# Optimization experiments

Hardware: AMD Instinct MI355X
Metric: run time of the kernel (lower is better)

## Reference

```python
import jax, jax.numpy as jnp
import numpy as np

D_IN, D_BIAS, H, DH = 256, 128, 8, 32

def _layernorm(x, w, b, eps=1e-5):
    mu = jnp.mean(x, axis=-1, keepdims=True)
    var = jnp.var(x, axis=-1, keepdims=True)
    return (x - mu) * jax.lax.rsqrt(var + eps) * w + b

def setup_inputs() -> dict:
    key = jax.random.key(0)
    ks = jax.random.split(key, 8)
    B, L = 1, 768
    x = jax.random.normal(ks[0], (B, L, D_IN), dtype=jnp.float32)
    bias = jax.random.normal(ks[1], (B, L, L, D_BIAS), dtype=jnp.float32)
    s_in = 1.0 / np.sqrt(D_IN)
    s_b = 1.0 / np.sqrt(D_BIAS)
    return {
        "x": x,
        "bias": bias,
        "ln_in_w": jnp.ones((D_IN,), jnp.float32),
        "ln_in_b": jnp.zeros((D_IN,), jnp.float32),
        "ln_b_w": jnp.ones((D_BIAS,), jnp.float32),
        "ln_b_b": jnp.zeros((D_BIAS,), jnp.float32),
        "Wq": jax.random.normal(ks[2], (D_IN, H * DH), jnp.float32) * s_in,
        "Wk": jax.random.normal(ks[3], (D_IN, H * DH), jnp.float32) * s_in,
        "Wv": jax.random.normal(ks[4], (D_IN, H * DH), jnp.float32) * s_in,
        "Wb": jax.random.normal(ks[5], (D_BIAS, H), jnp.float32) * s_b,
        "Wg": jax.random.normal(ks[6], (D_IN, H * DH), jnp.float32) * 0.02,
        "bg": jnp.ones((H * DH,), jnp.float32),
        "Wo": jax.random.normal(ks[7], (H * DH, D_IN), jnp.float32) * 0.02,
        "bo": jnp.zeros((D_IN,), jnp.float32),
    }

def reference(x, bias, ln_in_w, ln_in_b, ln_b_w, ln_b_b, Wq, Wk, Wv, Wb, Wg, bg, Wo, bo):
    B, L, _ = x.shape
    scaling = 1.0 / np.sqrt(DH)
    xn = _layernorm(x, ln_in_w, ln_in_b)            # (B,L,D_IN)
    bn = _layernorm(bias, ln_b_w, ln_b_b)           # (B,L,L,D_BIAS)
    q = (xn @ Wq).reshape(B, L, H, DH)
    k = (xn @ Wk).reshape(B, L, H, DH) * scaling
    v = (xn @ Wv).reshape(B, L, H, DH)
    b = bn @ Wb                                     # (B,L,L,H)
    gate = jax.nn.sigmoid(xn @ Wg + bg)             # (B,L,H*DH)
    attn = jnp.einsum('bqhd,bkhd->bqkh', q, k) + b  # (B,q,k,h)
    attn = jax.nn.softmax(attn, axis=2)             # softmax over key dim
    out = jnp.einsum('bqkh,bkhd->bqhd', attn, v).reshape(B, L, H * DH)
    out = gate * out
    return out @ Wo + bo
```

## Files before the change

### kernel.cpp

```cpp
#include <hip/hip_runtime.h>

#define LQ 768
#define DIN 256
#define DB 128
#define NH 8
#define DH 32

#define OFF_QB 0
#define OFF_KB (LQ*DIN)
#define OFF_VB (2*LQ*DIN)
#define OFF_GB (3*LQ*DIN)
#define OFF_W2 (4*LQ*DIN)
#define OFF_SC (OFF_W2 + DB*NH)
#define OFF_QK (OFF_SC + 16)

__global__ __launch_bounds__(256) void projsetup_kernel(
    const float* __restrict__ x, const float* __restrict__ lnw, const float* __restrict__ lnb,
    const float* __restrict__ Wq, const float* __restrict__ Wk, const float* __restrict__ Wv,
    const float* __restrict__ Wg, const float* __restrict__ bg,
    const float* __restrict__ lbw, const float* __restrict__ lbb, const float* __restrict__ Wb,
    float* __restrict__ qb, float* __restrict__ kb, float* __restrict__ vb, float* __restrict__ gb,
    float* __restrict__ W2, float* __restrict__ SC)
{
    const int tid = threadIdx.x;

    if (blockIdx.x == 192) {
        if (tid < 128) {
            const int d = tid, lane = d & 63, wv = d >> 6;
            float w = lbw[d], b = lbb[d];
            float pS[NH], pC[NH];
            #pragma unroll
            for (int h = 0; h < NH; h++) {
                float wb = Wb[d*NH + h];
                float w2 = w * wb;
                W2[d*NH + h] = w2;
                pS[h] = w2;
                pC[h] = b * wb;
            }
            #pragma unroll
            for (int m = 1; m <= 32; m <<= 1) {
                #pragma unroll
                for (int h = 0; h < NH; h++) { pS[h] += __shfl_xor(pS[h], m); pC[h] += __shfl_xor(pC[h], m); }
            }
            __shared__ float red[2][16];
            if (lane == 0) {
                #pragma unroll
                for (int h = 0; h < NH; h++) { red[wv][h] = pS[h]; red[wv][NH+h] = pC[h]; }
            }
            __syncthreads();
            if (d < 16) SC[d] = red[0][d] + red[1][d];
        }
        return;
    }

    const int lane = tid & 63, rr = tid >> 6;
    const int row = blockIdx.x * 4 + rr;
    __shared__ float xn[4][DIN];

    float4 xv = ((const float4*)x)[row * (DIN/4) + lane];
    float s  = xv.x + xv.y + xv.z + xv.w;
    float ss = xv.x*xv.x + xv.y*xv.y + xv.z*xv.z + xv.w*xv.w;
    #pragma unroll
    for (int m = 1; m <= 32; m <<= 1) { s += __shfl_xor(s, m); ss += __shfl_xor(ss, m); }
    float mu  = s * (1.0f/DIN);
    float inv = rsqrtf(ss * (1.0f/DIN) - mu*mu + 1e-5f);
    float4 wv4 = ((const float4*)lnw)[lane];
    float4 bv4 = ((const float4*)lnb)[lane];
    float4 r4;
    r4.x = (xv.x - mu)*inv*wv4.x + bv4.x;
    r4.y = (xv.y - mu)*inv*wv4.y + bv4.y;
    r4.z = (xv.z - mu)*inv*wv4.z + bv4.z;
    r4.w = (xv.w - mu)*inv*wv4.w + bv4.w;
    *((float4*)&xn[rr][lane*4]) = r4;
    __syncthreads();

    const int col = tid;
    float aq[4] = {0,0,0,0}, ak[4] = {0,0,0,0}, av[4] = {0,0,0,0}, ag[4] = {0,0,0,0};
    for (int i4 = 0; i4 < DIN/4; i4++) {
        float4 x0 = *((const float4*)&xn[0][i4*4]);
        float4 x1 = *((const float4*)&xn[1][i4*4]);
        float4 x2 = *((const float4*)&xn[2][i4*4]);
        float4 x3 = *((const float4*)&xn[3][i4*4]);
        const float* p0 = (const float*)&x0;
        const float* p1 = (const float*)&x1;
        const float* p2 = (const float*)&x2;
        const float* p3 = (const float*)&x3;
        #pragma unroll
        for (int e = 0; e < 4; e++) {
            const int i = i4*4 + e;
            float wq = Wq[i*DIN + col], wk = Wk[i*DIN + col];
            float wvv = Wv[i*DIN + col], wg = Wg[i*DIN + col];
            aq[0] = fmaf(p0[e], wq, aq[0]); aq[1] = fmaf(p1[e], wq, aq[1]);
            aq[2] = fmaf(p2[e], wq, aq[2]); aq[3] = fmaf(p3[e], wq, aq[3]);
            ak[0] = fmaf(p0[e], wk, ak[0]); ak[1] = fmaf(p1[e], wk, ak[1]);
            ak[2] = fmaf(p2[e], wk, ak[2]); ak[3] = fmaf(p3[e], wk, ak[3]);
            av[0] = fmaf(p0[e], wvv, av[0]); av[1] = fmaf(p1[e], wvv, av[1]);
            av[2] = fmaf(p2[e], wvv, av[2]); av[3] = fmaf(p3[e], wvv, av[3]);
            ag[0] = fmaf(p0[e], wg, ag[0]); ag[1] = fmaf(p1[e], wg, ag[1]);
            ag[2] = fmaf(p2[e], wg, ag[2]); ag[3] = fmaf(p3[e], wg, ag[3]);
        }
    }
    const float kscale = 0.17677669529663687f;
    float bgv = bg[col];
    #pragma unroll
    for (int r = 0; r < 4; r++) {
        const int orow = blockIdx.x*4 + r;
        qb[orow*DIN + col] = aq[r];
        kb[orow*DIN + col] = ak[r] * kscale;
        vb[orow*DIN + col] = av[r];
        gb[orow*DIN + col] = 1.0f/(1.0f + __expf(-(ag[r] + bgv)));
    }
}

__global__ __launch_bounds__(256) void qk_kernel(
    const float* __restrict__ qb, const float* __restrict__ kb, float* __restrict__ qkT)
{
    __shared__ float q_l[32*260];
    __shared__ float k_l[32*260];
    const int tid = threadIdx.x;
    const int bq = blockIdx.x, bk = blockIdx.y;

    {
        const int row = tid >> 3, cg = tid & 7;
        const float4* qs = (const float4*)(qb + (size_t)(bq*32 + row)*DIN + cg*32);
        const float4* ks = (const float4*)(kb + (size_t)(bk*32 + row)*DIN + cg*32);
        #pragma unroll
        for (int j = 0; j < 8; j++) {
            *(float4*)&q_l[row*260 + cg*32 + j*4] = qs[j];
            *(float4*)&k_l[row*260 + cg*32 + j*4] = ks[j];
        }
    }
    __syncthreads();

    const int tx = tid & 15, ty = tid >> 4;
    float acc[2][2][NH];
    #pragma unroll
    for (int a = 0; a < 2; a++)
        #pragma unroll
        for (int b = 0; b < 2; b++)
            #pragma unroll
            for (int h = 0; h < NH; h++) acc[a][b][h] = 0.f;

    #pragma unroll
    for (int d4 = 0; d4 < 64; d4++) {
        const int h = d4 >> 3;
        float4 q0 = *(const float4*)&q_l[(ty*2+0)*260 + d4*4];
        float4 q1 = *(const float4*)&q_l[(ty*2+1)*260 + d4*4];
        float4 k0 = *(const float4*)&k_l[(tx*2+0)*260 + d4*4];
        float4 k1 = *(const float4*)&k_l[(tx*2+1)*260 + d4*4];
        acc[0][0][h] = fmaf(q0.x,k0.x,acc[0][0][h]); acc[0][0][h] = fmaf(q0.y,k0.y,acc[0][0][h]);
        acc[0][0][h] = fmaf(q0.z,k0.z,acc[0][0][h]); acc[0][0][h] = fmaf(q0.w,k0.w,acc[0][0][h]);
        acc[0][1][h] = fmaf(q0.x,k1.x,acc[0][1][h]); acc[0][1][h] = fmaf(q0.y,k1.y,acc[0][1][h]);
        acc[0][1][h] = fmaf(q0.z,k1.z,acc[0][1][h]); acc[0][1][h] = fmaf(q0.w,k1.w,acc[0][1][h]);
        acc[1][0][h] = fmaf(q1.x,k0.x,acc[1][0][h]); acc[1][0][h] = fmaf(q1.y,k0.y,acc[1][0][h]);
        acc[1][0][h] = fmaf(q1.z,k0.z,acc[1][0][h]); acc[1][0][h] = fmaf(q1.w,k0.w,acc[1][0][h]);
        acc[1][1][h] = fmaf(q1.x,k1.x,acc[1][1][h]); acc[1][1][h] = fmaf(q1.y,k1.y,acc[1][1][h]);
        acc[1][1][h] = fmaf(q1.z,k1.z,acc[1][1][h]); acc[1][1][h] = fmaf(q1.w,k1.w,acc[1][1][h]);
    }

    #pragma unroll
    for (int a = 0; a < 2; a++)
        #pragma unroll
        for (int b = 0; b < 2; b++) {
            size_t base = ((size_t)(bq*32 + ty*2 + a)*LQ + (bk*32 + tx*2 + b))*NH;
            *(float4*)(qkT + base)     = make_float4(acc[a][b][0], acc[a][b][1], acc[a][b][2], acc[a][b][3]);
            *(float4*)(qkT + base + 4) = make_float4(acc[a][b][4], acc[a][b][5], acc[a][b][6], acc[a][b][7]);
        }
}

__global__ __launch_bounds__(256, 2) void fused_kernel(
    const float* __restrict__ bias, const float* __restrict__ W2g,
    const float* __restrict__ SCg, const float* __restrict__ qkT,
    const float* __restrict__ vbuf, const float* __restrict__ gbuf,
    const float* __restrict__ Wo, const float* __restrict__ bo,
    float* __restrict__ out)
{
    __shared__ float pT[NH][776];
    __shared__ float ao[DIN];
    __shared__ float isum[NH];

    const int tid  = threadIdx.x;
    const int q    = blockIdx.x;
    const int key8 = tid >> 3;
    const int dseg = tid & 7;

    float w2r[16][NH];
    {
        const float4* wp = (const float4*)(W2g + dseg*16*NH);
        #pragma unroll
        for (int j = 0; j < 16; j++) {
            float4 a = wp[j*2], b = wp[j*2+1];
            w2r[j][0]=a.x; w2r[j][1]=a.y; w2r[j][2]=a.z; w2r[j][3]=a.w;
            w2r[j][4]=b.x; w2r[j][5]=b.y; w2r[j][6]=b.z; w2r[j][7]=b.w;
        }
    }
    float Sh[NH], Ch[NH];
    #pragma unroll
    for (int h = 0; h < NH; h++) { Sh[h] = SCg[h]; Ch[h] = SCg[NH+h]; }

    const float* bsrc = bias + (size_t)q*LQ*DB + key8*DB + dseg*16;
    const float* qksrc = qkT + (size_t)q*LQ*NH + key8*NH + dseg;

    float4 va[4], vb4[4];

    #define LOADT(dst, t) {                                         \
        const float4* p = (const float4*)(bsrc + (size_t)(t)*4096); \
        dst[0]=p[0]; dst[1]=p[1]; dst[2]=p[2]; dst[3]=p[3]; }

    #define PROCESS(v, ht) {                                                    \
        float qk = qksrc[(ht)*32*NH];                                           \
        float s = 0.f, ss = 0.f;                                                \
        float acc[NH] = {0,0,0,0,0,0,0,0};                                      \
        _Pragma("unroll")                                                       \
        for (int j = 0; j < 4; j++) {                                           \
            _Pragma("unroll")                                                   \
            for (int e = 0; e < 4; e++) {                                       \
                float xv = (&v[j].x)[e];                                        \
                s += xv; ss = fmaf(xv, xv, ss);                                 \
                _Pragma("unroll")                                               \
                for (int h = 0; h < NH; h++)                                    \
                    acc[h] = fmaf(xv, w2r[j*4+e][h], acc[h]);                   \
            }                                                                   \
        }                                                                       \
        _Pragma("unroll")                                                       \
        for (int m = 1; m <= 4; m <<= 1) {                                      \
            s += __shfl_xor(s, m); ss += __shfl_xor(ss, m);                     \
            _Pragma("unroll")                                                   \
            for (int h = 0; h < NH; h++) acc[h] += __shfl_xor(acc[h], m);       \
        }                                                                       \
        float ah = acc[0], shh = Sh[0], chh = Ch[0];                            \
        _Pragma("unroll")                                                       \
        for (int h = 1; h < NH; h++) {                                          \
            bool psel = (dseg == h);                                            \
            ah = psel ? acc[h] : ah; shh = psel ? Sh[h] : shh;                  \
            chh = psel ? Ch[h] : chh;                                           \
        }                                                                       \
        float mu2  = s * (1.0f/DB);                                             \
        float inv2 = rsqrtf(ss * (1.0f/DB) - mu2*mu2 + 1e-5f);                  \
        float lo = fmaf(inv2, fmaf(-mu2, shh, ah), chh) + qk;                   \
        pT[dseg][(ht)*32 + key8] = lo; }

    LOADT(va, 0);
    for (int hp = 0; hp < 12; hp++) {
        LOADT(vb4, 2*hp + 1);
        PROCESS(va, 2*hp);
        if (hp < 11) LOADT(va, 2*hp + 2);
        PROCESS(vb4, 2*hp + 1);
    }
    #undef LOADT
    #undef PROCESS
    __syncthreads();

    {
        const int h = tid >> 5, l = tid & 31;
        float m = -1e30f;
        for (int i = l; i < LQ; i += 32) m = fmaxf(m, pT[h][i]);
        #pragma unroll
        for (int mm = 1; mm <= 16; mm <<= 1) m = fmaxf(m, __shfl_xor(m, mm));
        float sum = 0.f;
        for (int i = l; i < LQ; i += 32) {
            float e = __expf(pT[h][i] - m);
            pT[h][i] = e;
            sum += e;
        }
        #pragma unroll
        for (int mm = 1; mm <= 16; mm <<= 1) sum += __shfl_xor(sum, mm);
        if (l == 0) isum[h] = 1.0f / sum;
    }
    __syncthreads();

    {
        const int h = tid >> 5, d = tid & 31;
        const float* vp = vbuf + h*DH + d;
        float a = 0.f;
        for (int k4 = 0; k4 < LQ/4; k4++) {
            float4 p = *(const float4*)&pT[h][k4*4];
            a = fmaf(p.x, vp[(size_t)(k4*4+0)*DIN], a);
            a = fmaf(p.y, vp[(size_t)(k4*4+1)*DIN], a);
            a = fmaf(p.z, vp[(size_t)(k4*4+2)*DIN], a);
            a = fmaf(p.w, vp[(size_t)(k4*4+3)*DIN], a);
        }
        ao[tid] = a * isum[h] * gbuf[(size_t)q*DIN + tid];
    }
    __syncthreads();

    {
        float o = bo[tid];
        for (int i = 0; i < DIN; i++) o = fmaf(ao[i], Wo[i*DIN + tid], o);
        out[(size_t)q*DIN + tid] = o;
    }
}

extern "C" void kernel_launch(void* const* d_in, const int* in_sizes, int n_in,
                              void* d_out, int out_size, void* d_ws, size_t ws_size,
                              hipStream_t stream) {
    const float* x    = (const float*)d_in[0];
    const float* bias = (const float*)d_in[1];
    const float* lnw  = (const float*)d_in[2];
    const float* lnb  = (const float*)d_in[3];
    const float* lbw  = (const float*)d_in[4];
    const float* lbb  = (const float*)d_in[5];
    const float* Wq   = (const float*)d_in[6];
    const float* Wk   = (const float*)d_in[7];
    const float* Wv   = (const float*)d_in[8];
    const float* Wb   = (const float*)d_in[9];
    const float* Wg   = (const float*)d_in[10];
    const float* bg   = (const float*)d_in[11];
    const float* Wo   = (const float*)d_in[12];
    const float* bo   = (const float*)d_in[13];

    float* ws = (float*)d_ws;
    float* qb = ws + OFF_QB;
    float* kb = ws + OFF_KB;
    float* vb = ws + OFF_VB;
    float* gb = ws + OFF_GB;
    float* W2 = ws + OFF_W2;
    float* SC = ws + OFF_SC;
    float* qk = ws + OFF_QK;

    projsetup_kernel<<<193, 256, 0, stream>>>(x, lnw, lnb, Wq, Wk, Wv, Wg, bg,
                                              lbw, lbb, Wb, qb, kb, vb, gb, W2, SC);
    qk_kernel<<<dim3(24, 24), 256, 0, stream>>>(qb, kb, qk);
    fused_kernel<<<LQ, 256, 0, stream>>>(bias, W2, SC, qk, vb, gb, Wo, bo, (float*)d_out);
}
```

Before: 180.9 us.

## Fuse QK computation into main kernel and stage bias tiles through swizzled LDS

The separate qk_kernel and its global qkT buffer are removed. Each query block now computes its own row of Q·K scores from a transposed K buffer that the projection kernel writes. The bias layernorm/projection loop is restructured so each wave stages 16-key bias tiles into XOR-swizzled shared memory, prefetching the next tile in registers. W2 moves from registers to shared memory and the reduction is done across lane groups. This removes one launch and the qkT round trip through global memory, and should cut register pressure. The cost is more LDS traffic and extra per-block QK work, which re-reads the whole K matrix for every query.

```diff
diff --git a/kernel.cpp b/kernel.cpp
--- a/kernel.cpp
+++ b/kernel.cpp
@@ -7,19 +7,18 @@
 #define DH 32
 
 #define OFF_QB 0
-#define OFF_KB (LQ*DIN)
+#define OFF_KT (LQ*DIN)
 #define OFF_VB (2*LQ*DIN)
 #define OFF_GB (3*LQ*DIN)
 #define OFF_W2 (4*LQ*DIN)
 #define OFF_SC (OFF_W2 + DB*NH)
-#define OFF_QK (OFF_SC + 16)
 
 __global__ __launch_bounds__(256) void projsetup_kernel(
     const float* __restrict__ x, const float* __restrict__ lnw, const float* __restrict__ lnb,
     const float* __restrict__ Wq, const float* __restrict__ Wk, const float* __restrict__ Wv,
     const float* __restrict__ Wg, const float* __restrict__ bg,
     const float* __restrict__ lbw, const float* __restrict__ lbb, const float* __restrict__ Wb,
-    float* __restrict__ qb, float* __restrict__ kb, float* __restrict__ vb, float* __restrict__ gb,
+    float* __restrict__ qb, float* __restrict__ kT, float* __restrict__ vb, float* __restrict__ gb,
     float* __restrict__ W2, float* __restrict__ SC)
 {
     const int tid = threadIdx.x;
@@ -106,150 +105,143 @@
     for (int r = 0; r < 4; r++) {
         const int orow = blockIdx.x*4 + r;
         qb[orow*DIN + col] = aq[r];
-        kb[orow*DIN + col] = ak[r] * kscale;
         vb[orow*DIN + col] = av[r];
         gb[orow*DIN + col] = 1.0f/(1.0f + __expf(-(ag[r] + bgv)));
     }
+    *((float4*)&kT[col*LQ + blockIdx.x*4]) =
+        make_float4(ak[0]*kscale, ak[1]*kscale, ak[2]*kscale, ak[3]*kscale);
 }
 
-__global__ __launch_bounds__(256) void qk_kernel(
-    const float* __restrict__ qb, const float* __restrict__ kb, float* __restrict__ qkT)
+__global__ __launch_bounds__(256) void mega_kernel(
+    const float* __restrict__ bias, const float* __restrict__ W2g,
+    const float* __restrict__ SCg, const float* __restrict__ qbuf,
+    const float* __restrict__ kT, const float* __restrict__ vbuf,
+    const float* __restrict__ gbuf, const float* __restrict__ Wo,
+    const float* __restrict__ bo, float* __restrict__ out)
 {
-    __shared__ float q_l[32*260];
-    __shared__ float k_l[32*260];
-    const int tid = threadIdx.x;
-    const int bq = blockIdx.x, bk = blockIdx.y;
-
-    {
-        const int row = tid >> 3, cg = tid & 7;
-        const float4* qs = (const float4*)(qb + (size_t)(bq*32 + row)*DIN + cg*32);
-        const float4* ks = (const float4*)(kb + (size_t)(bk*32 + row)*DIN + cg*32);
-        #pragma unroll
-        for (int j = 0; j < 8; j++) {
-            *(float4*)&q_l[row*260 + cg*32 + j*4] = qs[j];
-            *(float4*)&k_l[row*260 + cg*32 + j*4] = ks[j];
-        }
-    }
-    __syncthreads();
-
-    const int tx = tid & 15, ty = tid >> 4;
-    float acc[2][2][NH];
-    #pragma unroll
-    for (int a = 0; a < 2; a++)
-        #pragma unroll
-        for (int b = 0; b < 2; b++)
-            #pragma unroll
-            for (int h = 0; h < NH; h++) acc[a][b][h] = 0.f;
-
-    #pragma unroll
-    for (int d4 = 0; d4 < 64; d4++) {
-        const int h = d4 >> 3;
-        float4 q0 = *(const float4*)&q_l[(ty*2+0)*260 + d4*4];
-        float4 q1 = *(const float4*)&q_l[(ty*2+1)*260 + d4*4];
-        float4 k0 = *(const float4*)&k_l[(tx*2+0)*260 + d4*4];
-        float4 k1 = *(const float4*)&k_l[(tx*2+1)*260 + d4*4];
-        acc[0][0][h] = fmaf(q0.x,k0.x,acc[0][0][h]); acc[0][0][h] = fmaf(q0.y,k0.y,acc[0][0][h]);
-        acc[0][0][h] = fmaf(q0.z,k0.z,acc[0][0][h]); acc[0][0][h] = fmaf(q0.w,k0.w,acc[0][0][h]);
-        acc[0][1][h] = fmaf(q0.x,k1.x,acc[0][1][h]); acc[0][1][h] = fmaf(q0.y,k1.y,acc[0][1][h]);
-        acc[0][1][h] = fmaf(q0.z,k1.z,acc[0][1][h]); acc[0][1][h] = fmaf(q0.w,k1.w,acc[0][1][h]);
-        acc[1][0][h] = fmaf(q1.x,k0.x,acc[1][0][h]); acc[1][0][h] = fmaf(q1.y,k0.y,acc[1][0][h]);
-        acc[1][0][h] = fmaf(q1.z,k0.z,acc[1][0][h]); acc[1][0][h] = fmaf(q1.w,k0.w,acc[1][0][h]);
-        acc[1][1][h] = fmaf(q1.x,k1.x,acc[1][1][h]); acc[1][1][h] = fmaf(q1.y,k1.y,acc[1][1][h]);
-        acc[1][1][h] = fmaf(q1.z,k1.z,acc[1][1][h]); acc[1][1][h] = fmaf(q1.w,k1.w,acc[1][1][h]);
-    }
-
-    #pragma unroll
-    for (int a = 0; a < 2; a++)
-        #pragma unroll
-        for (int b = 0; b < 2; b++) {
-            size_t base = ((size_t)(bq*32 + ty*2 + a)*LQ + (bk*32 + tx*2 + b))*NH;
-            *(float4*)(qkT + base)     = make_float4(acc[a][b][0], acc[a][b][1], acc[a][b][2], acc[a][b][3]);
-            *(float4*)(qkT + base + 4) = make_float4(acc[a][b][4], acc[a][b][5], acc[a][b][6], acc[a][b][7]);
-        }
-}
-
-__global__ __launch_bounds__(256, 2) void fused_kernel(
-    const float* __restrict__ bias, const float* __restrict__ W2g,
-    const float* __restrict__ SCg, const float* __restrict__ qkT,
-    const float* __restrict__ vbuf, const float* __restrict__ gbuf,
-    const float* __restrict__ Wo, const float* __restrict__ bo,
-    float* __restrict__ out)
-{
+    __shared__ float tiles[4][2048];
+    __shared__ float w2p[4*264];
     __shared__ float pT[NH][776];
     __shared__ float ao[DIN];
     __shared__ float isum[NH];
 
     const int tid  = threadIdx.x;
     const int q    = blockIdx.x;
-    const int key8 = tid >> 3;
-    const int dseg = tid & 7;
-
-    float w2r[16][NH];
-    {
-        const float4* wp = (const float4*)(W2g + dseg*16*NH);
-        #pragma unroll
-        for (int j = 0; j < 16; j++) {
-            float4 a = wp[j*2], b = wp[j*2+1];
-            w2r[j][0]=a.x; w2r[j][1]=a.y; w2r[j][2]=a.z; w2r[j][3]=a.w;
-            w2r[j][4]=b.x; w2r[j][5]=b.y; w2r[j][6]=b.z; w2r[j][7]=b.w;
-        }
-    }
+    const int w    = tid >> 6;
+    const int lane = tid & 63;
+    const int key  = lane & 15;
+    const int q4   = lane >> 4;
+
+    const char* gwave = (const char*)bias + ((size_t)q*LQ + w*192) * (DB*4);
+    float* tw = &tiles[w][0];
+
+    int soff[8];
+    #pragma unroll
+    for (int c = 0; c < 8; c++) {
+        int L = c*1024 + lane*16;
+        soff[c] = L ^ (((L >> 9) & 15) << 4);
+    }
+
+    float4 v[8];
+    #pragma unroll
+    for (int c = 0; c < 8; c++) v[c] = *(const float4*)(gwave + soff[c]);
+
+    for (int j = tid; j < 4*264; j += 256) {
+        int g = j / 264, rem = j - g*264;
+        w2p[j] = (rem < 256) ? W2g[g*256 + rem] : 0.0f;
+    }
+
+    if (tid < 192) {
+        float acc[4][NH];
+        #pragma unroll
+        for (int e = 0; e < 4; e++)
+            #pragma unroll
+            for (int h = 0; h < NH; h++) acc[e][h] = 0.f;
+        const float* qp = qbuf + (size_t)q*DIN;
+        #pragma unroll
+        for (int h = 0; h < NH; h++) {
+            #pragma unroll
+            for (int dd = 0; dd < DH; dd++) {
+                const int d = h*DH + dd;
+                float4 kv = *(const float4*)(kT + (size_t)d*LQ + tid*4);
+                float qa = qp[d];
+                acc[0][h] = fmaf(qa, kv.x, acc[0][h]);
+                acc[1][h] = fmaf(qa, kv.y, acc[1][h]);
+                acc[2][h] = fmaf(qa, kv.z, acc[2][h]);
+                acc[3][h] = fmaf(qa, kv.w, acc[3][h]);
+            }
+        }
+        #pragma unroll
+        for (int h = 0; h < NH; h++)
+            *(float4*)&pT[h][tid*4] = make_float4(acc[0][h], acc[1][h], acc[2][h], acc[3][h]);
+    }
+
+    asm volatile("s_waitcnt lgkmcnt(0)" ::: "memory");
+    __builtin_amdgcn_s_barrier();
+    asm volatile("" ::: "memory");
+
     float Sh[NH], Ch[NH];
     #pragma unroll
-    for (int h = 0; h < NH; h++) { Sh[h] = SCg[h]; Ch[h] = SCg[NH+h]; }
-
-    const float* bsrc = bias + (size_t)q*LQ*DB + key8*DB + dseg*16;
-    const float* qksrc = qkT + (size_t)q*LQ*NH + key8*NH + dseg;
-
-    float4 va[4], vb4[4];
-
-    #define LOADT(dst, t) {                                         \
-        const float4* p = (const float4*)(bsrc + (size_t)(t)*4096); \
-        dst[0]=p[0]; dst[1]=p[1]; dst[2]=p[2]; dst[3]=p[3]; }
-
-    #define PROCESS(v, ht) {                                                    \
-        float qk = qksrc[(ht)*32*NH];                                           \
-        float s = 0.f, ss = 0.f;                                                \
-        float acc[NH] = {0,0,0,0,0,0,0,0};                                      \
-        _Pragma("unroll")                                                       \
-        for (int j = 0; j < 4; j++) {                                           \
-            _Pragma("unroll")                                                   \
-            for (int e = 0; e < 4; e++) {                                       \
-                float xv = (&v[j].x)[e];                                        \
-                s += xv; ss = fmaf(xv, xv, ss);                                 \
-                _Pragma("unroll")                                               \
-                for (int h = 0; h < NH; h++)                                    \
-                    acc[h] = fmaf(xv, w2r[j*4+e][h], acc[h]);                   \
-            }                                                                   \
-        }                                                                       \
-        _Pragma("unroll")                                                       \
-        for (int m = 1; m <= 4; m <<= 1) {                                      \
-            s += __shfl_xor(s, m); ss += __shfl_xor(ss, m);                     \
-            _Pragma("unroll")                                                   \
-            for (int h = 0; h < NH; h++) acc[h] += __shfl_xor(acc[h], m);       \
-        }                                                                       \
-        float ah = acc[0], shh = Sh[0], chh = Ch[0];                            \
-        _Pragma("unroll")                                                       \
-        for (int h = 1; h < NH; h++) {                                          \
-            bool psel = (dseg == h);                                            \
-            ah = psel ? acc[h] : ah; shh = psel ? Sh[h] : shh;                  \
-            chh = psel ? Ch[h] : chh;                                           \
-        }                                                                       \
-        float mu2  = s * (1.0f/DB);                                             \
-        float inv2 = rsqrtf(ss * (1.0f/DB) - mu2*mu2 + 1e-5f);                  \
-        float lo = fmaf(inv2, fmaf(-mu2, shh, ah), chh) + qk;                   \
-        pT[dseg][(ht)*32 + key8] = lo; }
-
-    LOADT(va, 0);
-    for (int hp = 0; hp < 12; hp++) {
-        LOADT(vb4, 2*hp + 1);
-        PROCESS(va, 2*hp);
-        if (hp < 11) LOADT(va, 2*hp + 2);
-        PROCESS(vb4, 2*hp + 1);
-    }
-    #undef LOADT
-    #undef PROCESS
-    __syncthreads();
+    for (int h = 0; h < NH; h++) { Sh[h] = SCg[h]; Ch[h] = SCg[NH + h]; }
+
+    #pragma unroll
+    for (int c = 0; c < 8; c++) *(float4*)((char*)tw + c*1024 + lane*16) = v[c];
+    #pragma unroll
+    for (int c = 0; c < 8; c++) v[c] = *(const float4*)(gwave + 8192 + soff[c]);
+
+    const int rbase0 = ((key << 9) | (q4 << 7)) ^ (key << 4);
+    const float* wp = &w2p[q4*264];
+
+    #pragma unroll
+    for (int t = 0; t < 12; t++) {
+        float s = 0.f, ss = 0.f;
+        float acc[NH] = {0,0,0,0,0,0,0,0};
+        #pragma unroll
+        for (int j = 0; j < 8; j++) {
+            float4 bv = *(const float4*)((const char*)tw + (rbase0 ^ (j << 4)));
+            const float* wj = wp + j*32;
+            #pragma unroll
+            for (int e = 0; e < 4; e++) {
+                float xv = (&bv.x)[e];
+                s += xv; ss = fmaf(xv, xv, ss);
+                float4 w0 = *(const float4*)(wj + e*8);
+                float4 w1 = *(const float4*)(wj + e*8 + 4);
+                acc[0] = fmaf(xv, w0.x, acc[0]); acc[1] = fmaf(xv, w0.y, acc[1]);
+                acc[2] = fmaf(xv, w0.z, acc[2]); acc[3] = fmaf(xv, w0.w, acc[3]);
+                acc[4] = fmaf(xv, w1.x, acc[4]); acc[5] = fmaf(xv, w1.y, acc[5]);
+                acc[6] = fmaf(xv, w1.z, acc[6]); acc[7] = fmaf(xv, w1.w, acc[7]);
+            }
+        }
+        #pragma unroll
+        for (int m = 16; m <= 32; m <<= 1) {
+            s += __shfl_xor(s, m); ss += __shfl_xor(ss, m);
+            #pragma unroll
+            for (int h = 0; h < NH; h++) acc[h] += __shfl_xor(acc[h], m);
+        }
+        if (q4 == 0) {
+            float mu  = s * (1.0f/DB);
+            float inv = rsqrtf(ss * (1.0f/DB) - mu*mu + 1e-5f);
+            const int k = w*192 + t*16 + key;
+            #pragma unroll
+            for (int h = 0; h < NH; h++)
+                pT[h][k] += fmaf(inv, fmaf(-mu, Sh[h], acc[h]), Ch[h]);
+        }
+
+        if (t < 11) {
+            asm volatile("s_waitcnt lgkmcnt(0)" ::: "memory");
+            #pragma unroll
+            for (int c = 0; c < 8; c++) *(float4*)((char*)tw + c*1024 + lane*16) = v[c];
+            if (t < 10) {
+                const char* gs = gwave + (size_t)(t + 2)*8192;
+                #pragma unroll
+                for (int c = 0; c < 8; c++) v[c] = *(const float4*)(gs + soff[c]);
+            }
+        }
+    }
+
+    asm volatile("s_waitcnt lgkmcnt(0)" ::: "memory");
+    __builtin_amdgcn_s_barrier();
+    asm volatile("" ::: "memory");
 
     {
         const int h = tid >> 5, l = tid & 31;
@@ -311,15 +303,13 @@
 
     float* ws = (float*)d_ws;
     float* qb = ws + OFF_QB;
-    float* kb = ws + OFF_KB;
+    float* kT = ws + OFF_KT;
     float* vb = ws + OFF_VB;
     float* gb = ws + OFF_GB;
     float* W2 = ws + OFF_W2;
     float* SC = ws + OFF_SC;
-    float* qk = ws + OFF_QK;
 
     projsetup_kernel<<<193, 256, 0, stream>>>(x, lnw, lnb, Wq, Wk, Wv, Wg, bg,
-                                              lbw, lbb, Wb, qb, kb, vb, gb, W2, SC);
-    qk_kernel<<<dim3(24, 24), 256, 0, stream>>>(qb, kb, qk);
-    fused_kernel<<<LQ, 256, 0, stream>>>(bias, W2, SC, qk, vb, gb, Wo, bo, (float*)d_out);
+                                              lbw, lbb, Wb, qb, kT, vb, gb, W2, SC);
+    mega_kernel<<<LQ, 256, 0, stream>>>(bias, W2, SC, qb, kT, vb, gb, Wo, bo, (float*)d_out);
 }
```

After: 213.3 us. +17.9%, slower.
